# Kernel tuning notes

Hardware: AMD Instinct MI355X
Metric: run time of the kernel (lower is better)

The kernel has to match this reference:

```python
import jax, jax.numpy as jnp
import numpy as np

H = 16            # num_attention_heads
START_RATIO = 0.1
RECENT_RATIO = 0.4
THETA = 10000.0
CHUNK = 256       # hard-coded chunk_size in source
CLIP = 1e4        # nan_to_num posinf/neginf bound


def _rope_cos_sin(T, D, dtype):
    inv_freq = 1.0 / (THETA ** (jnp.arange(0, D, 2, dtype=jnp.float32) / D))
    freqs = jnp.arange(T, dtype=jnp.float32)[:, None] * inv_freq[None, :]  # [T, D/2]
    emb = jnp.concatenate([freqs, freqs], axis=-1)                          # [T, D]
    return jnp.cos(emb).astype(dtype), jnp.sin(emb).astype(dtype)


def _apply_rope(x, cos, sin):
    # x: [B,H,T,D]; cos/sin: [T,D] broadcast over B,H
    d = x.shape[-1] // 2
    rot = jnp.concatenate([-x[..., d:], x[..., :d]], axis=-1)
    return x * cos + rot * sin


def setup_inputs() -> dict:
    key = jax.random.key(0)
    k0, k1, k2, k3, k4 = jax.random.split(key, 5)
    B, T, Dm = 1, 2048, 2048
    scale = 1.0 / np.sqrt(Dm).astype(np.float32)
    return {
        "hidden_states": jax.random.normal(k0, (B, T, Dm), jnp.float32),
        "Wq": jax.random.normal(k1, (Dm, Dm), jnp.float32) * scale,
        "Wk": jax.random.normal(k2, (Dm, Dm), jnp.float32) * scale,
        "Wv": jax.random.normal(k3, (Dm, Dm), jnp.float32) * scale,
        "Wo": jax.random.normal(k4, (Dm, Dm), jnp.float32) * scale,
    }


def reference(hidden_states, Wq, Wk, Wv, Wo):
    B, T, Dm = hidden_states.shape
    D = Dm // H
    hs = jnp.nan_to_num(hidden_states, nan=0.0, posinf=CLIP, neginf=-CLIP)

    def proj(W):  # torch Linear: x @ W.T, then [B,T,H,D] -> [B,H,T,D]
        return (hs @ W.T).reshape(B, T, H, D).transpose(0, 2, 1, 3)

    q, k, v = proj(Wq), proj(Wk), proj(Wv)
    cos, sin = _rope_cos_sin(T, D, hs.dtype)
    q = _apply_rope(q, cos, sin)
    k = _apply_rope(k, cos, sin)

    # start+recent keep mask (past_key_value=None -> k_len == T)
    k_len = T
    sb = max(0, min(int(START_RATIO * k_len), k_len))
    rb = max(0, min(int(RECENT_RATIO * k_len), k_len - sb))
    pos = jnp.arange(k_len)
    keep = (pos < sb) | (pos >= k_len - rb)          # [K]

    MIN = jnp.finfo(hs.dtype).min
    scores = jnp.einsum('bhqd,bhkd->bhqk', q, k) / jnp.sqrt(jnp.asarray(D, hs.dtype))
    scores = jnp.where(keep, scores, MIN)
    probs = jax.nn.softmax(scores, axis=-1)          # [B,H,T,K]

    # CaM merge of evicted V into recent window, driven by the LAST query row.
    evict = k_len - rb                               # static python int
    last = probs[..., -1, :]                         # [B,H,K]
    mean_attn = last[..., evict + 1:].mean(axis=-1) + 1e-6
    p = jnp.clip(last[..., evict] / mean_attn, 0.0, 1.0)
    p = jnp.nan_to_num(p, nan=0.0, posinf=1.0, neginf=0.0)
    u = jax.random.uniform(jax.random.key(42), p.shape, p.dtype)
    bern = (u < p).astype(v.dtype)                   # [B,H]
    v_e = v[..., evict, :] * bern[..., None] / rb    # [B,H,D]
    v_merged = v.at[..., evict + 1:, :].add(v_e[..., None, :])

    # Chunked loop effect: only the last chunk's AV uses merged V.
    last_start = ((T - 1) // CHUNK) * CHUNK
    out_pre = jnp.einsum('bhqk,bhkd->bhqd', probs[:, :, :last_start], v)
    out_last = jnp.einsum('bhqk,bhkd->bhqd', probs[:, :, last_start:], v_merged)
    out = jnp.concatenate([out_pre, out_last], axis=2)   # [B,H,T,D]

    out = out.transpose(0, 2, 1, 3).reshape(B, T, Dm) @ Wo.T
    return jnp.nan_to_num(out, nan=0.0, posinf=CLIP, neginf=-CLIP)
```

## Files before the change

kernel.cpp:

```cpp
#include <hip/hip_runtime.h>
#include <stdint.h>

#define T_SEQ 2048
#define DM    2048
#define NH    16
#define HD    128
#define SB    204
#define EV    1229
#define RB    819
#define NRECF 818.0f
#define LAST_START 1792
#define SCALE 0.08838834764831845f

typedef __attribute__((ext_vector_type(8))) short short8;
typedef __attribute__((ext_vector_type(4))) short short4v;
typedef __attribute__((ext_vector_type(4))) float f32x4;

__device__ __forceinline__ unsigned short f2bf(float f) {
  uint32_t u = __float_as_uint(f);
  u += 0x7fffu + ((u >> 16) & 1u);
  return (unsigned short)(u >> 16);
}
__device__ __forceinline__ float bf2f(unsigned short s) {
  return __uint_as_float(((uint32_t)s) << 16);
}
__device__ __forceinline__ void gload16(const void* g, void* l) {
  __builtin_amdgcn_global_load_lds((const __attribute__((address_space(1))) void*)g,
                                   (__attribute__((address_space(3))) void*)l,
                                   16, 0, 0);
}
__device__ __forceinline__ float n2n(float v) {
  if (isnan(v)) return 0.0f;
  if (isinf(v)) return v > 0.0f ? 10000.0f : -10000.0f;
  return v;
}

__global__ __launch_bounds__(256) void cvt_kernel(
    const float* __restrict__ hs, const float* __restrict__ wq,
    const float* __restrict__ wk, const float* __restrict__ wv,
    const float* __restrict__ wo, unsigned short* __restrict__ hsb,
    unsigned short* __restrict__ wqb, unsigned short* __restrict__ wkb,
    unsigned short* __restrict__ wvb, unsigned short* __restrict__ wob,
    float* __restrict__ cst, float* __restrict__ snt) {
  if (blockIdx.x >= 20480) {
    int idx = (blockIdx.x - 20480) * 256 + threadIdx.x;
    int t = idx >> 6, i = idx & 63;
    float inv = (float)exp(-(double)i * log(10000.0) / 64.0);
    float ang = (float)t * inv;
    cst[idx] = (float)cos((double)ang);
    snt[idx] = (float)sin((double)ang);
    return;
  }
  int gid = blockIdx.x * 256 + threadIdx.x;
  int region = gid >> 20;
  int off4 = (gid & 1048575) * 4;
  const float* src; unsigned short* dst;
  switch (region) {
    case 0: src = hs; dst = hsb; break;
    case 1: src = wq; dst = wqb; break;
    case 2: src = wk; dst = wkb; break;
    case 3: src = wv; dst = wvb; break;
    default: src = wo; dst = wob; break;
  }
  float4 v = *(const float4*)(src + off4);
  if (region == 0) { v.x = n2n(v.x); v.y = n2n(v.y); v.z = n2n(v.z); v.w = n2n(v.w); }
  ushort4 o;
  o.x = f2bf(v.x); o.y = f2bf(v.y); o.z = f2bf(v.z); o.w = f2bf(v.w);
  *(ushort4*)(dst + off4) = o;
}

__device__ __forceinline__ void gemm_mainloop64(
    const unsigned short* __restrict__ A, const unsigned short* __restrict__ B,
    unsigned short* As, unsigned short* Bs, int m0, int n0, int k0, int ksteps,
    int tid, f32x4 (&acc)[4][4]) {
  int w = tid >> 6, lane = tid & 63;
  int wm = w >> 1, wn = w & 1;
  int q4 = lane >> 4, r = lane & 15;
  f32x4 zero = {0.f, 0.f, 0.f, 0.f};
  #pragma unroll
  for (int mi = 0; mi < 4; mi++)
    #pragma unroll
    for (int ni = 0; ni < 4; ni++) acc[mi][ni] = zero;
  int srow = w * 32 + (lane >> 3);
  int swz = ((lane & 7) ^ (lane >> 3)) * 16;
  const char* Ag = (const char*)(A + (size_t)(m0 + srow) * DM) + swz + k0 * 2;
  const char* Bg = (const char*)(B + (size_t)(n0 + srow) * DM) + swz + k0 * 2;
  unsigned short* Asl = As + w * 2048;
  unsigned short* Bsl = Bs + w * 2048;
  for (int s = 0; s < ksteps; s++) {
    __syncthreads();
    #pragma unroll
    for (int g = 0; g < 4; g++) {
      gload16(Ag + g * (8 * DM * 2), Asl + g * 512);
      gload16(Bg + g * (8 * DM * 2), Bsl + g * 512);
    }
    Ag += 128; Bg += 128;
    __syncthreads();
    #pragma unroll
    for (int kh = 0; kh < 2; kh++) {
      int pcs = ((kh * 4 + q4) ^ (r & 7)) * 8;
      short8 a[4], b[4];
      #pragma unroll
      for (int mi = 0; mi < 4; mi++)
        a[mi] = *(const short8*)(As + (wm * 64 + mi * 16 + r) * 64 + pcs);
      #pragma unroll
      for (int ni = 0; ni < 4; ni++)
        b[ni] = *(const short8*)(Bs + ((ni & 1) * 64 + wn * 32 + (ni >> 1) * 16 + r) * 64 + pcs);
      #pragma unroll
      for (int mi = 0; mi < 4; mi++)
        #pragma unroll
        for (int ni = 0; ni < 4; ni++)
          acc[mi][ni] = __builtin_amdgcn_mfma_f32_16x16x32_bf16(a[mi], b[ni], acc[mi][ni], 0, 0, 0);
    }
  }
}

__global__ __launch_bounds__(256, 3) void gemm_qkv_kernel(
    const unsigned short* __restrict__ hsb, const unsigned short* __restrict__ wqb,
    const unsigned short* __restrict__ wkb, const unsigned short* __restrict__ wvb,
    const float* __restrict__ cst, const float* __restrict__ snt,
    unsigned short* __restrict__ qbf, unsigned short* __restrict__ kbf,
    unsigned short* __restrict__ vbT) {
  __shared__ __align__(16) unsigned short LDSBUF[17408];
  unsigned short* As = LDSBUF;
  unsigned short* Bs = LDSBUF + 8192;
  int y = blockIdx.y;
  int z, mi;
  if (y < 16)      { z = 0; mi = y; }
  else if (y < 25) { z = 1; mi = y - 16; }
  else             { z = 2; mi = y - 25; }
  if (z) mi = (mi < 2) ? mi : mi + 7;
  const unsigned short* B = (z == 0) ? wqb : (z == 1) ? wkb : wvb;
  int m0 = mi * 128, n0 = blockIdx.x * 128;
  f32x4 acc[4][4];
  gemm_mainloop64(hsb, B, As, Bs, m0, n0, 0, DM / 64, threadIdx.x, acc);
  int tid = threadIdx.x, w = tid >> 6, lane = tid & 63;
  int wm = w >> 1, wn = w & 1, q4 = lane >> 4, r = lane & 15;
  int h = n0 >> 7;
  if (z < 2) {
    unsigned short* dst = (z == 0) ? qbf : kbf;
    #pragma unroll
    for (int mj = 0; mj < 4; mj++)
      #pragma unroll
      for (int p = 0; p < 2; p++) {
        int d = wn * 32 + p * 16 + r;
        #pragma unroll
        for (int g = 0; g < 4; g++) {
          int t = m0 + wm * 64 + mj * 16 + q4 * 4 + g;
          float c = cst[t * 64 + d], s = snt[t * 64 + d];
          float x0 = acc[mj][2 * p][g], x1 = acc[mj][2 * p + 1][g];
          dst[((size_t)h * T_SEQ + t) * HD + d]      = f2bf(x0 * c - x1 * s);
          dst[((size_t)h * T_SEQ + t) * HD + d + 64] = f2bf(x1 * c + x0 * s);
        }
      }
  } else {
    __syncthreads();
    #pragma unroll
    for (int mj = 0; mj < 4; mj++)
      #pragma unroll
      for (int ni = 0; ni < 4; ni++) {
        int c = (ni & 1) * 64 + wn * 32 + (ni >> 1) * 16 + r;
        int tl = wm * 64 + mj * 16 + q4 * 4;
        short4v pv;
        pv[0] = (short)f2bf(acc[mj][ni][0]);
        pv[1] = (short)f2bf(acc[mj][ni][1]);
        pv[2] = (short)f2bf(acc[mj][ni][2]);
        pv[3] = (short)f2bf(acc[mj][ni][3]);
        *(short4v*)(LDSBUF + c * 136 + tl) = pv;
      }
    __syncthreads();
    int d = tid >> 1, th = tid & 1;
    unsigned short* gdst = vbT + ((size_t)h * HD + d) * T_SEQ + m0 + th * 64;
    const unsigned short* lsrc = LDSBUF + d * 136 + th * 64;
    #pragma unroll
    for (int j = 0; j < 8; j++)
      *(short8*)(gdst + j * 8) = *(const short8*)(lsrc + j * 8);
  }
}

__device__ __forceinline__ void attn_body(
    int kb, const unsigned short* Kt, const unsigned short* Vt,
    const unsigned short* indv, unsigned short* Psw,
    const short8 (&aq)[4], f32x4 (&o)[8], f32x4& o9, float (&evf)[4],
    int q4, int r) {
  f32x4 zero = {0.f, 0.f, 0.f, 0.f};
  int rsw = (r >> 1) & 3;
  f32x4 s0 = zero, s1 = zero;
  #pragma unroll
  for (int c = 0; c < 4; c++) {
    int pc = ((c * 4 + q4) ^ r) * 8;
    short8 bk0 = *(const short8*)(Kt + r * 128 + pc);
    short8 bk1 = *(const short8*)(Kt + (16 + r) * 128 + pc);
    s0 = __builtin_amdgcn_mfma_f32_16x16x32_bf16(aq[c], bk0, s0, 0, 0, 0);
    s1 = __builtin_amdgcn_mfma_f32_16x16x32_bf16(aq[c], bk1, s1, 0, 0, 0);
  }
  int kg0 = kb + r, kg1 = kb + 16 + r;
  bool keep0 = (kg0 < SB) || (kg0 >= EV);
  bool keep1 = (kg1 < SB) || (kg1 >= EV);
  #pragma unroll
  for (int g = 0; g < 4; g++) {
    float p0 = keep0 ? __expf(fmaf(s0[g], SCALE, -8.0f)) : 0.0f;
    float p1 = keep1 ? __expf(fmaf(s1[g], SCALE, -8.0f)) : 0.0f;
    if (kb == 1216 && kg0 == EV) evf[g] = p0;
    int row = q4 * 4 + g;
    int psw = (row >> 1) & 3;
    Psw[row * 32 + (((r >> 3) ^ psw) * 8) + (r & 7)]       = f2bf(p0);
    Psw[row * 32 + ((((r >> 3) + 2) ^ psw) * 8) + (r & 7)] = f2bf(p1);
  }
  short8 pa = *(const short8*)(Psw + r * 32 + (q4 ^ rsw) * 8);
  #pragma unroll
  for (int ni = 0; ni < 8; ni++) {
    short8 bv = *(const short8*)(Vt + (ni * 16 + r) * 32 + (q4 ^ rsw) * 8);
    o[ni] = __builtin_amdgcn_mfma_f32_16x16x32_bf16(pa, bv, o[ni], 0, 0, 0);
  }
  short8 bind = *(const short8*)(indv + r * 32 + (q4 ^ rsw) * 8);
  o9 = __builtin_amdgcn_mfma_f32_16x16x32_bf16(pa, bind, o9, 0, 0, 0);
}

__global__ __launch_bounds__(256, 2) void attn_kernel(
    const unsigned short* __restrict__ qbf, const unsigned short* __restrict__ kbf,
    const unsigned short* __restrict__ vbT, unsigned short* __restrict__ atb,
    float* __restrict__ attnf_s, float* __restrict__ Ssum, float* __restrict__ lst) {
  __shared__ __align__(16) unsigned short KtS[2][2][4096];
  __shared__ __align__(16) unsigned short VtS[2][2][4096];
  __shared__ __align__(16) unsigned short Ps[4][512];
  __shared__ __align__(16) unsigned short Ind[3 * 512];
  int tid = threadIdx.x, w = tid >> 6, lane = tid & 63;
  int q4 = lane >> 4, r = lane & 15;
  int h = blockIdx.y;
  int qb = blockIdx.x * 64 + w * 16;

  for (int idx = tid; idx < 3 * 512; idx += 256) {
    int v = idx >> 9, n = (idx >> 5) & 15, j = idx & 31;
    float val = 0.f;
    if (n == 0) val = 1.f;
    else if (n == 1) val = (v == 1) ? (j >= 14 ? 1.f : 0.f) : (v == 2 ? 1.f : 0.f);
    Ind[v * 512 + n * 32 + (((j >> 3) ^ ((n >> 1) & 3)) * 8) + (j & 7)] = f2bf(val);
  }

  short8 aq[4];
  {
    const unsigned short* qrow = qbf + ((size_t)h * T_SEQ + qb + r) * HD;
    #pragma unroll
    for (int c = 0; c < 4; c++) aq[c] = *(const short8*)(qrow + c * 32 + q4 * 8);
  }
  f32x4 zero = {0.f, 0.f, 0.f, 0.f};
  f32x4 o[8], o9;
  #pragma unroll
  for (int ni = 0; ni < 8; ni++) o[ni] = zero;
  o9 = zero;
  float evf[4] = {0.f, 0.f, 0.f, 0.f};

  const char* Kbase = (const char*)(kbf + (size_t)h * T_SEQ * HD);
  int krow0 = w * 8 + q4, krow1 = krow0 + 4;
  const char* Kg0 = Kbase + krow0 * 256 + ((r ^ (krow0 & 15)) * 16);
  const char* Kg1 = Kbase + krow1 * 256 + ((r ^ (krow1 & 15)) * 16);
  const char* Vbase = (const char*)(vbT + (size_t)h * HD * T_SEQ);
  int vsrc = ((lane & 3) ^ ((lane >> 3) & 3)) * 16;
  const char* Vg0 = Vbase + (size_t)(w * 32 + (lane >> 2)) * 4096 + vsrc;
  const char* Vg1 = Vg0 + 16 * 4096;

  auto issue_chunk = [&](int ci, int db) {
    int kb = (ci < 4) ? ci * 64 : 1216 + (ci - 4) * 64;
    gload16(Kg0 + kb * 256,         &KtS[db][0][w * 1024]);
    gload16(Kg1 + kb * 256,         &KtS[db][0][w * 1024 + 512]);
    gload16(Kg0 + (kb + 32) * 256,  &KtS[db][1][w * 1024]);
    gload16(Kg1 + (kb + 32) * 256,  &KtS[db][1][w * 1024 + 512]);
    gload16(Vg0 + kb * 2,           &VtS[db][0][w * 1024]);
    gload16(Vg1 + kb * 2,           &VtS[db][0][w * 1024 + 512]);
    gload16(Vg0 + (kb + 32) * 2,    &VtS[db][1][w * 1024]);
    gload16(Vg1 + (kb + 32) * 2,    &VtS[db][1][w * 1024 + 512]);
  };

  issue_chunk(0, 0);
  for (int ci = 0; ci < 17; ci++) {
    int db = ci & 1;
    int kb = (ci < 4) ? ci * 64 : 1216 + (ci - 4) * 64;
    const unsigned short* indA = Ind + ((ci < 4) ? 0 : (ci == 4) ? 512 : 1024);
    const unsigned short* indB = Ind + ((ci < 4) ? 0 : 1024);
    __syncthreads();
    if (ci < 16) issue_chunk(ci + 1, db ^ 1);
    attn_body(kb,      KtS[db][0], VtS[db][0], indA, &Ps[w][0], aq, o, o9, evf, q4, r);
    attn_body(kb + 32, KtS[db][1], VtS[db][1], indB, &Ps[w][0], aq, o, o9, evf, q4, r);
  }

  float invl[4], srn[4], evn[4];
  #pragma unroll
  for (int g = 0; g < 4; g++) {
    float l  = __shfl(o9[g], lane & 48, 64);
    float sr = __shfl(o9[g], (lane & 48) | 1, 64);
    float ev = __shfl(evf[g], (lane & 48) | 13, 64);
    invl[g] = 1.0f / l;
    srn[g] = sr * invl[g];
    evn[g] = ev * invl[g];
  }
  if (blockIdx.x < (LAST_START / 64)) {
    #pragma unroll
    for (int ni = 0; ni < 8; ni++)
      #pragma unroll
      for (int g = 0; g < 4; g++)
        atb[(size_t)(qb + q4 * 4 + g) * DM + h * HD + ni * 16 + r] = f2bf(o[ni][g] * invl[g]);
  } else {
    #pragma unroll
    for (int ni = 0; ni < 8; ni++)
      #pragma unroll
      for (int g = 0; g < 4; g++)
        attnf_s[(size_t)(qb - LAST_START + q4 * 4 + g) * DM + h * HD + ni * 16 + r] = o[ni][g] * invl[g];
  }
  if (r == 0) {
    #pragma unroll
    for (int g = 0; g < 4; g++) {
      int t = qb + q4 * 4 + g;
      if (t >= LAST_START) Ssum[h * 256 + (t - LAST_START)] = srn[g];
      if (t == T_SEQ - 1) { lst[h * 2] = evn[g]; lst[h * 2 + 1] = srn[g]; }
    }
  }
}

__device__ __forceinline__ void tf_round(uint32_t& x0, uint32_t& x1, int rot) {
  x0 += x1;
  x1 = (x1 << rot) | (x1 >> (32 - rot));
  x1 ^= x0;
}
__device__ __forceinline__ float bern_scale(int hh, const float* lst) {
  const uint32_t k0 = 0u, k1 = 42u, k2 = 0x1BD11BDAu ^ k0 ^ k1;
  uint32_t x0 = (uint32_t)(hh & 7), x1 = (uint32_t)((hh & 7) + 8);
  x0 += k0; x1 += k1;
  tf_round(x0, x1, 13); tf_round(x0, x1, 15); tf_round(x0, x1, 26); tf_round(x0, x1, 6);
  x0 += k1; x1 += k2 + 1u;
  tf_round(x0, x1, 17); tf_round(x0, x1, 29); tf_round(x0, x1, 16); tf_round(x0, x1, 24);
  x0 += k2; x1 += k0 + 2u;
  tf_round(x0, x1, 13); tf_round(x0, x1, 15); tf_round(x0, x1, 26); tf_round(x0, x1, 6);
  x0 += k0; x1 += k1 + 3u;
  tf_round(x0, x1, 17); tf_round(x0, x1, 29); tf_round(x0, x1, 16); tf_round(x0, x1, 24);
  x0 += k1; x1 += k2 + 4u;
  tf_round(x0, x1, 13); tf_round(x0, x1, 15); tf_round(x0, x1, 26); tf_round(x0, x1, 6);
  x0 += k2; x1 += k0 + 5u;
  uint32_t bits = (hh < 8) ? x0 : x1;
  float u = __uint_as_float((bits >> 9) | 0x3f800000u) - 1.0f;
  float evp = lst[hh * 2], srp = lst[hh * 2 + 1];
  float mean = srp * (1.0f / NRECF) + 1e-6f;
  float p = evp / mean;
  p = fminf(fmaxf(p, 0.0f), 1.0f);
  if (!(p == p)) p = 0.0f;
  return (u < p) ? (1.0f / (float)RB) : 0.0f;
}

__global__ __launch_bounds__(256) void fixup_kernel(
    const float* __restrict__ attnf_s, const float* __restrict__ Ssum,
    const float* __restrict__ lst, const unsigned short* __restrict__ vbT,
    unsigned short* __restrict__ atb) {
  int idx = blockIdx.x * 256 + threadIdx.x;
  int t2 = idx >> 11, n = idx & 2047;
  int h = n >> 7, d = n & 127;
  float bsc = bern_scale(h, lst);
  float v = attnf_s[idx];
  v += Ssum[h * 256 + t2] * bsc * bf2f(vbT[((size_t)h * HD + d) * T_SEQ + EV]);
  atb[(size_t)(t2 + LAST_START) * DM + n] = f2bf(v);
}

__global__ __launch_bounds__(256, 3) void gemm_out_kernel(
    const unsigned short* __restrict__ atb, const unsigned short* __restrict__ wob,
    float* __restrict__ part0, float* __restrict__ part1) {
  __shared__ __align__(16) unsigned short LDSBUF[16384];
  unsigned short* As = LDSBUF;
  unsigned short* Bs = LDSBUF + 8192;
  int m0 = blockIdx.y * 128, n0 = blockIdx.x * 128;
  int kz = blockIdx.z;
  float* part = kz ? part1 : part0;
  f32x4 acc[4][4];
  gemm_mainloop64(atb, wob, As, Bs, m0, n0, kz * 1024, 16, threadIdx.x, acc);
  int tid = threadIdx.x, w = tid >> 6, lane = tid & 63;
  int wm = w >> 1, wn = w & 1, q4 = lane >> 4, r = lane & 15;
  #pragma unroll
  for (int mi = 0; mi < 4; mi++)
    #pragma unroll
    for (int ni = 0; ni < 4; ni++) {
      int c = n0 + (ni & 1) * 64 + wn * 32 + (ni >> 1) * 16 + r;
      #pragma unroll
      for (int g = 0; g < 4; g++) {
        int t = m0 + wm * 64 + mi * 16 + q4 * 4 + g;
        part[(size_t)t * DM + c] = acc[mi][ni][g];
      }
    }
}

__global__ __launch_bounds__(256) void add_kernel(
    const float* __restrict__ p0, const float* __restrict__ p1, float* __restrict__ out) {
  int i4 = (blockIdx.x * 256 + threadIdx.x) * 4;
  float4 a = *(const float4*)(p0 + i4);
  float4 b = *(const float4*)(p1 + i4);
  float4 o;
  o.x = n2n(a.x + b.x); o.y = n2n(a.y + b.y);
  o.z = n2n(a.z + b.z); o.w = n2n(a.w + b.w);
  *(float4*)(out + i4) = o;
}

extern "C" void kernel_launch(void* const* d_in, const int* in_sizes, int n_in,
                              void* d_out, int out_size, void* d_ws, size_t ws_size,
                              hipStream_t stream) {
  const float* hs = (const float*)d_in[0];
  const float* Wq = (const float*)d_in[1];
  const float* Wk = (const float*)d_in[2];
  const float* Wv = (const float*)d_in[3];
  const float* Wo = (const float*)d_in[4];
  char* ws = (char*)d_ws;
  const size_t MB = 1024 * 1024;
  unsigned short* hsb = (unsigned short*)(ws + 0);
  unsigned short* wqb = (unsigned short*)(ws + 8 * MB);
  unsigned short* wkb = (unsigned short*)(ws + 16 * MB);
  unsigned short* wvb = (unsigned short*)(ws + 24 * MB);
  unsigned short* wob = (unsigned short*)(ws + 32 * MB);
  unsigned short* qbf = (unsigned short*)(ws + 40 * MB);
  unsigned short* kbf = (unsigned short*)(ws + 48 * MB);
  unsigned short* vbT = (unsigned short*)(ws + 56 * MB);
  unsigned short* atb = (unsigned short*)(ws + 64 * MB);
  float* attnf_s = (float*)(ws + 72 * MB);
  float* part0 = (float*)(ws + 74 * MB);
  float* part1 = (float*)(ws + 90 * MB);
  float* cst = (float*)(ws + 106 * MB);
  float* snt = (float*)(ws + 106 * MB + 524288);
  float* Ssum = (float*)(ws + 107 * MB);
  float* lst = (float*)(ws + 107 * MB + 16384);

  cvt_kernel<<<20992, 256, 0, stream>>>(hs, Wq, Wk, Wv, Wo, hsb, wqb, wkb, wvb, wob, cst, snt);
  gemm_qkv_kernel<<<dim3(16, 34), 256, 0, stream>>>(hsb, wqb, wkb, wvb, cst, snt, qbf, kbf, vbT);
  attn_kernel<<<dim3(32, 16), 256, 0, stream>>>(qbf, kbf, vbT, atb, attnf_s, Ssum, lst);
  fixup_kernel<<<2048, 256, 0, stream>>>(attnf_s, Ssum, lst, vbT, atb);
  gemm_out_kernel<<<dim3(16, 16, 2), 256, 0, stream>>>(atb, wob, part0, part1);
  add_kernel<<<4096, 256, 0, stream>>>(part0, part1, (float*)d_out);
}
```

Before: 242.5 us.

## Fold CaM V-merge correction into post-GEMM rank-16 update and drop split-K

```diff
diff --git a/kernel.cpp b/kernel.cpp
--- a/kernel.cpp
+++ b/kernel.cpp
@@ -220,7 +220,7 @@
 __global__ __launch_bounds__(256, 2) void attn_kernel(
     const unsigned short* __restrict__ qbf, const unsigned short* __restrict__ kbf,
     const unsigned short* __restrict__ vbT, unsigned short* __restrict__ atb,
-    float* __restrict__ attnf_s, float* __restrict__ Ssum, float* __restrict__ lst) {
+    float* __restrict__ Ssum, float* __restrict__ lst) {
   __shared__ __align__(16) unsigned short KtS[2][2][4096];
   __shared__ __align__(16) unsigned short VtS[2][2][4096];
   __shared__ __align__(16) unsigned short Ps[4][512];
@@ -294,19 +294,11 @@
     srn[g] = sr * invl[g];
     evn[g] = ev * invl[g];
   }
-  if (blockIdx.x < (LAST_START / 64)) {
-    #pragma unroll
-    for (int ni = 0; ni < 8; ni++)
-      #pragma unroll
-      for (int g = 0; g < 4; g++)
-        atb[(size_t)(qb + q4 * 4 + g) * DM + h * HD + ni * 16 + r] = f2bf(o[ni][g] * invl[g]);
-  } else {
-    #pragma unroll
-    for (int ni = 0; ni < 8; ni++)
-      #pragma unroll
-      for (int g = 0; g < 4; g++)
-        attnf_s[(size_t)(qb - LAST_START + q4 * 4 + g) * DM + h * HD + ni * 16 + r] = o[ni][g] * invl[g];
-  }
+  #pragma unroll
+  for (int ni = 0; ni < 8; ni++)
+    #pragma unroll
+    for (int g = 0; g < 4; g++)
+      atb[(size_t)(qb + q4 * 4 + g) * DM + h * HD + ni * 16 + r] = f2bf(o[ni][g] * invl[g]);
   if (r == 0) {
     #pragma unroll
     for (int g = 0; g < 4; g++) {
@@ -315,6 +307,61 @@
       if (t == T_SEQ - 1) { lst[h * 2] = evn[g]; lst[h * 2 + 1] = srn[g]; }
     }
   }
+}
+
+__global__ __launch_bounds__(256, 2) void gemm_out_kernel(
+    const unsigned short* __restrict__ atb, const unsigned short* __restrict__ wob,
+    float* __restrict__ out) {
+  __shared__ __align__(16) unsigned short As[4096];
+  __shared__ __align__(16) unsigned short Bs[8192];
+  int tid = threadIdx.x, w = tid >> 6, lane = tid & 63;
+  int q4 = lane >> 4, r = lane & 15;
+  int m0 = blockIdx.y * 64, n0 = blockIdx.x * 128;
+  f32x4 zero = {0.f, 0.f, 0.f, 0.f};
+  f32x4 acc[4][2];
+  #pragma unroll
+  for (int mi = 0; mi < 4; mi++) { acc[mi][0] = zero; acc[mi][1] = zero; }
+  int swz = ((lane & 7) ^ (lane >> 3)) * 16;
+  const char* Ag = (const char*)(atb + (size_t)(m0 + w * 16 + (lane >> 3)) * DM) + swz;
+  const char* Bg = (const char*)(wob + (size_t)(n0 + w * 32 + (lane >> 3)) * DM) + swz;
+  unsigned short* Asl = As + w * 1024;
+  unsigned short* Bsl = Bs + w * 2048;
+  for (int s = 0; s < 32; s++) {
+    __syncthreads();
+    gload16(Ag,               Asl);
+    gload16(Ag + 8 * DM * 2,  Asl + 512);
+    #pragma unroll
+    for (int g = 0; g < 4; g++)
+      gload16(Bg + g * (8 * DM * 2), Bsl + g * 512);
+    Ag += 128; Bg += 128;
+    __syncthreads();
+    #pragma unroll
+    for (int kh = 0; kh < 2; kh++) {
+      int pcs = ((kh * 4 + q4) ^ (r & 7)) * 8;
+      short8 a[4], b[2];
+      #pragma unroll
+      for (int mi = 0; mi < 4; mi++)
+        a[mi] = *(const short8*)(As + (mi * 16 + r) * 64 + pcs);
+      b[0] = *(const short8*)(Bs + (w * 32 + r) * 64 + pcs);
+      b[1] = *(const short8*)(Bs + (w * 32 + 16 + r) * 64 + pcs);
+      #pragma unroll
+      for (int mi = 0; mi < 4; mi++) {
+        acc[mi][0] = __builtin_amdgcn_mfma_f32_16x16x32_bf16(a[mi], b[0], acc[mi][0], 0, 0, 0);
+        acc[mi][1] = __builtin_amdgcn_mfma_f32_16x16x32_bf16(a[mi], b[1], acc[mi][1], 0, 0, 0);
+      }
+    }
+  }
+  #pragma unroll
+  for (int mi = 0; mi < 4; mi++)
+    #pragma unroll
+    for (int ni = 0; ni < 2; ni++) {
+      int c = n0 + w * 32 + ni * 16 + r;
+      #pragma unroll
+      for (int g = 0; g < 4; g++) {
+        int t = m0 + mi * 16 + q4 * 4 + g;
+        out[(size_t)t * DM + c] = n2n(acc[mi][ni][g]);
+      }
+    }
 }
 
 __device__ __forceinline__ void tf_round(uint32_t& x0, uint32_t& x1, int rot) {
@@ -346,54 +393,34 @@
   return (u < p) ? (1.0f / (float)RB) : 0.0f;
 }
 
-__global__ __launch_bounds__(256) void fixup_kernel(
-    const float* __restrict__ attnf_s, const float* __restrict__ Ssum,
+__global__ __launch_bounds__(256) void fix_kernel(
+    float* __restrict__ out, const float* __restrict__ Ssum,
     const float* __restrict__ lst, const unsigned short* __restrict__ vbT,
-    unsigned short* __restrict__ atb) {
-  int idx = blockIdx.x * 256 + threadIdx.x;
-  int t2 = idx >> 11, n = idx & 2047;
-  int h = n >> 7, d = n & 127;
-  float bsc = bern_scale(h, lst);
-  float v = attnf_s[idx];
-  v += Ssum[h * 256 + t2] * bsc * bf2f(vbT[((size_t)h * HD + d) * T_SEQ + EV]);
-  atb[(size_t)(t2 + LAST_START) * DM + n] = f2bf(v);
-}
-
-__global__ __launch_bounds__(256, 3) void gemm_out_kernel(
-    const unsigned short* __restrict__ atb, const unsigned short* __restrict__ wob,
-    float* __restrict__ part0, float* __restrict__ part1) {
-  __shared__ __align__(16) unsigned short LDSBUF[16384];
-  unsigned short* As = LDSBUF;
-  unsigned short* Bs = LDSBUF + 8192;
-  int m0 = blockIdx.y * 128, n0 = blockIdx.x * 128;
-  int kz = blockIdx.z;
-  float* part = kz ? part1 : part0;
-  f32x4 acc[4][4];
-  gemm_mainloop64(atb, wob, As, Bs, m0, n0, kz * 1024, 16, threadIdx.x, acc);
-  int tid = threadIdx.x, w = tid >> 6, lane = tid & 63;
-  int wm = w >> 1, wn = w & 1, q4 = lane >> 4, r = lane & 15;
-  #pragma unroll
-  for (int mi = 0; mi < 4; mi++)
-    #pragma unroll
-    for (int ni = 0; ni < 4; ni++) {
-      int c = n0 + (ni & 1) * 64 + wn * 32 + (ni >> 1) * 16 + r;
-      #pragma unroll
-      for (int g = 0; g < 4; g++) {
-        int t = m0 + wm * 64 + mi * 16 + q4 * 4 + g;
-        part[(size_t)t * DM + c] = acc[mi][ni][g];
-      }
-    }
-}
-
-__global__ __launch_bounds__(256) void add_kernel(
-    const float* __restrict__ p0, const float* __restrict__ p1, float* __restrict__ out) {
-  int i4 = (blockIdx.x * 256 + threadIdx.x) * 4;
-  float4 a = *(const float4*)(p0 + i4);
-  float4 b = *(const float4*)(p1 + i4);
-  float4 o;
-  o.x = n2n(a.x + b.x); o.y = n2n(a.y + b.y);
-  o.z = n2n(a.z + b.z); o.w = n2n(a.w + b.w);
-  *(float4*)(out + i4) = o;
+    const unsigned short* __restrict__ wob) {
+  __shared__ float vev[NH * HD];
+  int tid = threadIdx.x;
+  for (int i = tid; i < NH * HD; i += 256)
+    vev[i] = bf2f(vbT[((size_t)i) * T_SEQ + EV]);
+  __syncthreads();
+  int cb = blockIdx.x & 7, tb = blockIdx.x >> 3;
+  int c = cb * 256 + tid;
+  float coef[NH];
+  #pragma unroll
+  for (int h = 0; h < NH; h++) {
+    float g = 0.f;
+    const unsigned short* wrow = wob + (size_t)c * DM + h * HD;
+    #pragma unroll 4
+    for (int d = 0; d < HD; d++)
+      g += vev[h * HD + d] * bf2f(wrow[d]);
+    coef[h] = bern_scale(h, lst) * g;
+  }
+  #pragma unroll 4
+  for (int t2 = tb * 32; t2 < tb * 32 + 32; t2++) {
+    float add = 0.f;
+    #pragma unroll
+    for (int h = 0; h < NH; h++) add += Ssum[h * 256 + t2] * coef[h];
+    out[(size_t)(LAST_START + t2) * DM + c] += add;
+  }
 }
 
 extern "C" void kernel_launch(void* const* d_in, const int* in_sizes, int n_in,
@@ -415,18 +442,14 @@
   unsigned short* kbf = (unsigned short*)(ws + 48 * MB);
   unsigned short* vbT = (unsigned short*)(ws + 56 * MB);
   unsigned short* atb = (unsigned short*)(ws + 64 * MB);
-  float* attnf_s = (float*)(ws + 72 * MB);
-  float* part0 = (float*)(ws + 74 * MB);
-  float* part1 = (float*)(ws + 90 * MB);
-  float* cst = (float*)(ws + 106 * MB);
-  float* snt = (float*)(ws + 106 * MB + 524288);
-  float* Ssum = (float*)(ws + 107 * MB);
-  float* lst = (float*)(ws + 107 * MB + 16384);
+  float* cst = (float*)(ws + 72 * MB);
+  float* snt = (float*)(ws + 72 * MB + 524288);
+  float* Ssum = (float*)(ws + 73 * MB);
+  float* lst = (float*)(ws + 73 * MB + 16384);
 
   cvt_kernel<<<20992, 256, 0, stream>>>(hs, Wq, Wk, Wv, Wo, hsb, wqb, wkb, wvb, wob, cst, snt);
   gemm_qkv_kernel<<<dim3(16, 34), 256, 0, stream>>>(hsb, wqb, wkb, wvb, cst, snt, qbf, kbf, vbT);
-  attn_kernel<<<dim3(32, 16), 256, 0, stream>>>(qbf, kbf, vbT, atb, attnf_s, Ssum, lst);
-  fixup_kernel<<<2048, 256, 0, stream>>>(attnf_s, Ssum, lst, vbT, atb);
-  gemm_out_kernel<<<dim3(16, 16, 2), 256, 0, stream>>>(atb, wob, part0, part1);
-  add_kernel<<<4096, 256, 0, stream>>>(part0, part1, (float*)d_out);
-}
+  attn_kernel<<<dim3(32, 16), 256, 0, stream>>>(qbf, kbf, vbT, atb, Ssum, lst);
+  gemm_out_kernel<<<dim3(16, 32), 256, 0, stream>>>(atb, wob, (float*)d_out);
+  fix_kernel<<<64, 256, 0, stream>>>((float*)d_out, Ssum, lst, vbT, wob);
+}
```

Measured after the change: 309.2 us. 27.5% more time.
